# Performance work log

Hardware: AMD Instinct MI355X
Metric: run time of the kernel (lower is better)

The kernel has to match this reference:

```python
import jax, jax.numpy as jnp
import numpy as np

B, M, D = 2048, 40, 64          # batch, num fields, embedding dim
HIDDEN = [128, 128, 128]        # CIN layer sizes


def setup_inputs() -> dict:
    key = jax.random.key(0)
    kx, k0, k1, k2 = jax.random.split(key, 4)
    x = jax.random.normal(kx, (B, M, D), dtype=jnp.float32)
    # torch.rand -> uniform [0, 1)
    W0 = jax.random.uniform(k0, (M, M, HIDDEN[0]), dtype=jnp.float32)
    W1 = jax.random.uniform(k1, (M, HIDDEN[0], HIDDEN[1]), dtype=jnp.float32)
    W2 = jax.random.uniform(k2, (M, HIDDEN[1], HIDDEN[2]), dtype=jnp.float32)
    return {"x": x, "W0": W0, "W1": W1, "W2": W2}


def _cin_forward(x, Ws):
    # x: [b, m, d]. Each layer k:
    #   x_next[b, l, d] = sum_{m, h} x0[b, m, d] * x_k[b, h, d] * W_k[m, h, l]
    # which equals the torch 'bil,bjl->bjil' outer product followed by
    # 'bijk,ijl->bkl' + transpose, but expressed as one fused contraction
    # (opt_einsum picks a path avoiding the worst intermediate).
    ps = []
    xk = x  # [b, H_k, d], H_0 = m
    for W in Ws:
        x_next = jnp.einsum('bmd,bhd,mhl->bld', x, xk, W)  # [b, L_k, d]
        ps.append(jnp.sum(x_next, axis=2))                  # [b, L_k]
        xk = x_next
    return jnp.concatenate(ps, axis=1)                      # [b, sum(L_k)]


def reference(x, W0, W1, W2):
    return _cin_forward(x, (W0, W1, W2))
```

## Files before the change

kernel.cpp:

```cpp
#include <hip/hip_runtime.h>
#include <hip/hip_bf16.h>
#include <cstdint>

#define BATCH 2048
#define MF    40
#define DDIM  64
#define LDIM  128
#define ROWS  (BATCH * DDIM)

typedef __attribute__((ext_vector_type(4)))  short    short4_t;
typedef __attribute__((ext_vector_type(8)))  short    short8;
typedef __attribute__((ext_vector_type(8)))  __bf16   bf16x8;
typedef __attribute__((ext_vector_type(2)))  float    floatx2;
typedef __attribute__((ext_vector_type(16))) float    floatx16;

__device__ __forceinline__ unsigned short f32_to_bf16(float f) {
    union { float f; uint32_t u; } v; v.f = f;
    uint32_t u = v.u;
    uint32_t r = (u + 0x7fffu + ((u >> 16) & 1u)) >> 16;
    return (unsigned short)r;
}

__device__ __forceinline__ void barrier_raw() {
    asm volatile("s_barrier" ::: "memory");
}
__device__ __forceinline__ void lgkmwait0() {
    asm volatile("s_waitcnt lgkmcnt(0)" ::: "memory");
}
template <int N> __device__ __forceinline__ void vmwait() {
    if constexpr (N == 0)  asm volatile("s_waitcnt vmcnt(0)"  ::: "memory");
    if constexpr (N == 4)  asm volatile("s_waitcnt vmcnt(4)"  ::: "memory");
    if constexpr (N == 6)  asm volatile("s_waitcnt vmcnt(6)"  ::: "memory");
    if constexpr (N == 10) asm volatile("s_waitcnt vmcnt(10)" ::: "memory");
}

__global__ void k_wprep_all(const float* __restrict__ W0, const float* __restrict__ W1,
                            const float* __restrict__ W2,
                            unsigned short* __restrict__ W0t,
                            unsigned short* __restrict__ W1t,
                            unsigned short* __restrict__ W2t) {
    int bi = blockIdx.x;
    const float* W; unsigned short* Wt; int KK, H;
    if (bi < 640)       { W = W0; Wt = W0t; KK = 4; H = 40; }
    else if (bi < 1920) { bi -= 640;  W = W1; Wt = W1t; KK = 8; H = 128; }
    else                { bi -= 1920; W = W2; Wt = W2t; KK = 8; H = 128; }
    int lane = threadIdx.x;
    int cb = bi & 3;
    int mkk = bi >> 2;
    int kk = mkk % KK, m = mkk / KK;
    int l = cb * 32 + (lane & 31);
    int hbase = kk * 16 + (lane >> 5) * 8;
    unsigned short o[8];
#pragma unroll
    for (int j = 0; j < 8; ++j) {
        int h = hbase + j;
        float v = (h < H) ? W[((size_t)m * H + h) * LDIM + l] : 0.f;
        o[j] = f32_to_bf16(v);
    }
    *(short8*)(Wt + (((size_t)(m * KK + kk) * 4 + cb) * 64 + lane) * 8) = *(const short8*)o;
}

template <int KK>
__device__ __forceinline__ void layer_loop(
    const unsigned short* __restrict__ Wt,
    const float* __restrict__ x, int b,
    int lane, int hf, int r31, int cbg0, int cbg1,
    unsigned short* slabf,
    bf16x8 (&xk)[2][8], floatx16 (&acc)[2][2])
{
    constexpr int UPM  = KK / 4;
    constexpr int NU   = MF * UPM;
    constexpr int GATE = (KK == 8) ? 10 : 6;

    auto stage = [&](int uu) {
        int u = uu < NU ? uu : NU - 1;
        const unsigned short* src = Wt + (size_t)u * 8192;
        const int tid = threadIdx.x;
#pragma unroll
        for (int it = 0; it < 4; ++it) {
            int c = it * 256 + tid;
            __builtin_amdgcn_global_load_lds(
                (const __attribute__((address_space(1))) uint32_t*)(src + (size_t)c * 8),
                (__attribute__((address_space(3))) uint32_t*)(&slabf[(size_t)(u & 3) * 8192 + (size_t)c * 8]),
                16, 0, 0);
        }
    };
    auto ldfrag = [&](int u, int frag, int cb) {
        return __builtin_bit_cast(bf16x8, *(const short8*)(
            &slabf[(size_t)(u & 3) * 8192 + ((size_t)(frag * 4 + cb) * 64 + lane) * 8]));
    };

    acc[0][0] = floatx16{}; acc[0][1] = floatx16{};
    acc[1][0] = floatx16{}; acc[1][1] = floatx16{};

    vmwait<0>();
    stage(0); stage(1); stage(2);
    vmwait<4>();
    barrier_raw();

    bf16x8 bbuf[2][2];
#pragma unroll
    for (int p = 0; p < 2; ++p) {
        bbuf[p][0] = ldfrag(0, p, cbg0);
        bbuf[p][1] = ldfrag(0, p, cbg1);
    }

    float s0v = 0.f, s1v = 0.f;

#pragma unroll 1
    for (int m = 0; m < MF; ++m) {
        floatx16 P[2][2] = {};
#pragma unroll
        for (int kk = 0; kk < KK; ++kk) {
            if (kk % 4 == 0) {
                barrier_raw();
                asm volatile("s_setprio 1");
                if (kk == 0) {
                    const float* sp = x + ((size_t)b * MF + m) * DDIM + r31;
                    s0v = sp[0];
                    s1v = sp[32];
                }
                stage(m * UPM + kk / 4 + 3);
            }
            const int slot = kk & 1;
            P[0][0] = __builtin_amdgcn_mfma_f32_32x32x16_bf16(bbuf[slot][0], xk[0][kk], P[0][0], 0, 0, 0);
            P[1][0] = __builtin_amdgcn_mfma_f32_32x32x16_bf16(bbuf[slot][0], xk[1][kk], P[1][0], 0, 0, 0);
            P[0][1] = __builtin_amdgcn_mfma_f32_32x32x16_bf16(bbuf[slot][1], xk[0][kk], P[0][1], 0, 0, 0);
            P[1][1] = __builtin_amdgcn_mfma_f32_32x32x16_bf16(bbuf[slot][1], xk[1][kk], P[1][1], 0, 0, 0);
            {
                const int j  = kk + 2;
                int mm = m + ((j >= KK) ? 1 : 0);
                if (mm > MF - 1) mm = MF - 1;
                const int jj = (j >= KK) ? (j - KK) : j;
                const int u  = mm * UPM + jj / 4;
                bbuf[slot][0] = ldfrag(u, jj % 4, cbg0);
                bbuf[slot][1] = ldfrag(u, jj % 4, cbg1);
            }
            if (kk % 4 == 3) vmwait<GATE>();
        }
        asm volatile("s_setprio 0");
#pragma unroll
        for (int t = 0; t < 2; ++t) {
            const float sv = (t == 0) ? s0v : s1v;
            floatx2 s2 = {sv, sv};
#pragma unroll
            for (int cbp = 0; cbp < 2; ++cbp) {
                floatx2*       A = (floatx2*)&acc[t][cbp];
                const floatx2* Q = (const floatx2*)&P[t][cbp];
#pragma unroll
                for (int i = 0; i < 8; ++i) A[i] += s2 * Q[i];
            }
        }
    }
}

__global__ __launch_bounds__(256, 2) void k_cin(
    const float* __restrict__ x,
    const unsigned short* __restrict__ W0t,
    const unsigned short* __restrict__ W1t,
    const unsigned short* __restrict__ W2t,
    float* __restrict__ out)
{
    __shared__ unsigned short slab[4][8192];
    unsigned short* slabf = &slab[0][0];

    const int tid  = threadIdx.x;
    const int lane = tid & 63, wave = tid >> 6;
    const int hf   = lane >> 5, r31 = lane & 31;
    const int rowhalf = wave >> 1, colhalf = wave & 1;
    const int b = blockIdx.x * 2 + rowhalf;
    const int cbg0 = colhalf * 2, cbg1 = colhalf * 2 + 1;

    bf16x8   xk[2][8];
    floatx16 acc[2][2];

    auto write_ps = [&](int OFF) {
#pragma unroll
        for (int cbp = 0; cbp < 2; ++cbp) {
#pragma unroll
            for (int j = 0; j < 16; ++j) {
                float v = acc[0][cbp][j] + acc[1][cbp][j];
                v += __shfl_xor(v, 16);
                v += __shfl_xor(v, 8);
                v += __shfl_xor(v, 4);
                v += __shfl_xor(v, 2);
                v += __shfl_xor(v, 1);
                if (r31 == 0)
                    out[(size_t)b * 384 + OFF + (colhalf * 2 + cbp) * 32 +
                        (j & 3) + 8 * (j >> 2) + 4 * hf] = v;
            }
        }
    };

    auto exchange = [&]() {
        vmwait<0>();
        barrier_raw();
#pragma unroll
        for (int t = 0; t < 2; ++t)
#pragma unroll
            for (int cbp = 0; cbp < 2; ++cbp)
#pragma unroll
                for (int g = 0; g < 4; ++g) {
                    unsigned short o[4];
#pragma unroll
                    for (int i = 0; i < 4; ++i) o[i] = f32_to_bf16(acc[t][cbp][g * 4 + i]);
                    const int kk  = colhalf * 4 + cbp * 2 + (g >> 1);
                    const int hfr = g & 1;
                    *(short4_t*)(&slabf[(size_t)rowhalf * 8192 +
                        ((size_t)(t * 8 + kk) * 64 + hfr * 32 + r31) * 8 + 4 * hf]) =
                        *(const short4_t*)o;
                }
        lgkmwait0();
        barrier_raw();
#pragma unroll
        for (int t = 0; t < 2; ++t)
#pragma unroll
            for (int kk = 0; kk < 8; ++kk)
                xk[t][kk] = __builtin_bit_cast(bf16x8, *(const short8*)(
                    &slabf[(size_t)rowhalf * 8192 + ((size_t)(t * 8 + kk) * 64 + lane) * 8]));
        lgkmwait0();
        barrier_raw();
    };

#pragma unroll
    for (int t = 0; t < 2; ++t)
#pragma unroll
        for (int kk = 0; kk < 4; ++kk) {
            unsigned short tmp[8];
#pragma unroll
            for (int j = 0; j < 8; ++j) {
                int h = kk * 16 + hf * 8 + j;
                float v = (h < MF) ? x[((size_t)b * MF + h) * DDIM + t * 32 + r31] : 0.f;
                tmp[j] = f32_to_bf16(v);
            }
            xk[t][kk] = __builtin_bit_cast(bf16x8, *(const short8*)tmp);
        }

    layer_loop<4>(W0t, x, b, lane, hf, r31, cbg0, cbg1, slabf, xk, acc);
    write_ps(0);
    exchange();

    layer_loop<8>(W1t, x, b, lane, hf, r31, cbg0, cbg1, slabf, xk, acc);
    write_ps(128);
    exchange();

    layer_loop<8>(W2t, x, b, lane, hf, r31, cbg0, cbg1, slabf, xk, acc);
    write_ps(256);
}

extern "C" void kernel_launch(void* const* d_in, const int* in_sizes, int n_in,
                              void* d_out, int out_size, void* d_ws, size_t ws_size,
                              hipStream_t stream) {
    const float* x  = (const float*)d_in[0];
    const float* W0 = (const float*)d_in[1];
    const float* W1 = (const float*)d_in[2];
    const float* W2 = (const float*)d_in[3];
    float* out = (float*)d_out;

    char* ws = (char*)d_ws;
    size_t off = 0;
    auto alloc = [&](size_t bytes) -> void* {
        void* p = ws + off;
        off += (bytes + 255) & ~(size_t)255;
        return p;
    };
    unsigned short* W0t = (unsigned short*)alloc((size_t)MF * 4 * 2048 * 2);
    unsigned short* W1t = (unsigned short*)alloc((size_t)MF * 8 * 2048 * 2);
    unsigned short* W2t = (unsigned short*)alloc((size_t)MF * 8 * 2048 * 2);

    k_wprep_all<<<3200, 64, 0, stream>>>(W0, W1, W2, W0t, W1t, W2t);
    k_cin<<<ROWS / 128, 256, 0, stream>>>(x, W0t, W1t, W2t, out);
}
```

Measured before the change: 434.1 us.

## Split work to one batch per block across d-halves, shrink LDS staging

Each block now handles a single batch row, with its four waves split over the two 32-wide d-halves and two column groups, where before each block covered two batch rows. Per-wave accumulators and xk registers are halved and the LDS weight slab shrinks to 4096 entries per stage, so launch bounds can rise to four blocks per CU. Partial sums from the two d-halves are combined through a small shared scratch before the output is written. Each block still streams the full weights, so weight traffic through L2 per batch row doubles, and pipeline waits and barriers now come twice as often per unit of MFMA work.

```diff
diff --git a/kernel.cpp b/kernel.cpp
--- a/kernel.cpp
+++ b/kernel.cpp
@@ -6,7 +6,6 @@
 #define MF    40
 #define DDIM  64
 #define LDIM  128
-#define ROWS  (BATCH * DDIM)
 
 typedef __attribute__((ext_vector_type(4)))  short    short4_t;
 typedef __attribute__((ext_vector_type(8)))  short    short8;
@@ -28,10 +27,9 @@
     asm volatile("s_waitcnt lgkmcnt(0)" ::: "memory");
 }
 template <int N> __device__ __forceinline__ void vmwait() {
-    if constexpr (N == 0)  asm volatile("s_waitcnt vmcnt(0)"  ::: "memory");
-    if constexpr (N == 4)  asm volatile("s_waitcnt vmcnt(4)"  ::: "memory");
-    if constexpr (N == 6)  asm volatile("s_waitcnt vmcnt(6)"  ::: "memory");
-    if constexpr (N == 10) asm volatile("s_waitcnt vmcnt(10)" ::: "memory");
+    if constexpr (N == 0) asm volatile("s_waitcnt vmcnt(0)" ::: "memory");
+    if constexpr (N == 2) asm volatile("s_waitcnt vmcnt(2)" ::: "memory");
+    if constexpr (N == 3) asm volatile("s_waitcnt vmcnt(3)" ::: "memory");
 }
 
 __global__ void k_wprep_all(const float* __restrict__ W0, const float* __restrict__ W1,
@@ -63,39 +61,37 @@
 template <int KK>
 __device__ __forceinline__ void layer_loop(
     const unsigned short* __restrict__ Wt,
-    const float* __restrict__ x, int b,
-    int lane, int hf, int r31, int cbg0, int cbg1,
+    const float* __restrict__ x, int b, int t,
+    int lane, int cbg0, int cbg1,
     unsigned short* slabf,
-    bf16x8 (&xk)[2][8], floatx16 (&acc)[2][2])
+    bf16x8 (&xk)[8], floatx16 (&acc)[2])
 {
-    constexpr int UPM  = KK / 4;
-    constexpr int NU   = MF * UPM;
-    constexpr int GATE = (KK == 8) ? 10 : 6;
+    constexpr int UPM = KK / 2;
+    constexpr int NU  = MF * UPM;
 
     auto stage = [&](int uu) {
         int u = uu < NU ? uu : NU - 1;
-        const unsigned short* src = Wt + (size_t)u * 8192;
+        const unsigned short* src = Wt + (size_t)u * 4096;
         const int tid = threadIdx.x;
 #pragma unroll
-        for (int it = 0; it < 4; ++it) {
+        for (int it = 0; it < 2; ++it) {
             int c = it * 256 + tid;
             __builtin_amdgcn_global_load_lds(
                 (const __attribute__((address_space(1))) uint32_t*)(src + (size_t)c * 8),
-                (__attribute__((address_space(3))) uint32_t*)(&slabf[(size_t)(u & 3) * 8192 + (size_t)c * 8]),
+                (__attribute__((address_space(3))) uint32_t*)(&slabf[(u & 3) * 4096 + c * 8]),
                 16, 0, 0);
         }
     };
-    auto ldfrag = [&](int u, int frag, int cb) {
+    auto ldfrag = [&](int u, int f, int cb) {
         return __builtin_bit_cast(bf16x8, *(const short8*)(
-            &slabf[(size_t)(u & 3) * 8192 + ((size_t)(frag * 4 + cb) * 64 + lane) * 8]));
-    };
-
-    acc[0][0] = floatx16{}; acc[0][1] = floatx16{};
-    acc[1][0] = floatx16{}; acc[1][1] = floatx16{};
+            &slabf[(u & 3) * 4096 + ((f * 4 + cb) * 64 + lane) * 8]));
+    };
+
+    acc[0] = floatx16{}; acc[1] = floatx16{};
 
     vmwait<0>();
     stage(0); stage(1); stage(2);
-    vmwait<4>();
+    vmwait<2>();
     barrier_raw();
 
     bf16x8 bbuf[2][2];
@@ -105,146 +101,136 @@
         bbuf[p][1] = ldfrag(0, p, cbg1);
     }
 
-    float s0v = 0.f, s1v = 0.f;
+    float sv = 0.f;
 
 #pragma unroll 1
     for (int m = 0; m < MF; ++m) {
-        floatx16 P[2][2] = {};
+        floatx16 P[2] = {};
 #pragma unroll
         for (int kk = 0; kk < KK; ++kk) {
-            if (kk % 4 == 0) {
+            if ((kk & 1) == 0) {
                 barrier_raw();
                 asm volatile("s_setprio 1");
-                if (kk == 0) {
-                    const float* sp = x + ((size_t)b * MF + m) * DDIM + r31;
-                    s0v = sp[0];
-                    s1v = sp[32];
-                }
-                stage(m * UPM + kk / 4 + 3);
+                if (kk == 0)
+                    sv = x[((size_t)b * MF + m) * DDIM + t * 32 + (lane & 31)];
+                stage(m * UPM + (kk >> 1) + 3);
             }
             const int slot = kk & 1;
-            P[0][0] = __builtin_amdgcn_mfma_f32_32x32x16_bf16(bbuf[slot][0], xk[0][kk], P[0][0], 0, 0, 0);
-            P[1][0] = __builtin_amdgcn_mfma_f32_32x32x16_bf16(bbuf[slot][0], xk[1][kk], P[1][0], 0, 0, 0);
-            P[0][1] = __builtin_amdgcn_mfma_f32_32x32x16_bf16(bbuf[slot][1], xk[0][kk], P[0][1], 0, 0, 0);
-            P[1][1] = __builtin_amdgcn_mfma_f32_32x32x16_bf16(bbuf[slot][1], xk[1][kk], P[1][1], 0, 0, 0);
+            P[0] = __builtin_amdgcn_mfma_f32_32x32x16_bf16(bbuf[slot][0], xk[kk], P[0], 0, 0, 0);
+            P[1] = __builtin_amdgcn_mfma_f32_32x32x16_bf16(bbuf[slot][1], xk[kk], P[1], 0, 0, 0);
             {
                 const int j  = kk + 2;
                 int mm = m + ((j >= KK) ? 1 : 0);
                 if (mm > MF - 1) mm = MF - 1;
                 const int jj = (j >= KK) ? (j - KK) : j;
-                const int u  = mm * UPM + jj / 4;
-                bbuf[slot][0] = ldfrag(u, jj % 4, cbg0);
-                bbuf[slot][1] = ldfrag(u, jj % 4, cbg1);
-            }
-            if (kk % 4 == 3) vmwait<GATE>();
+                const int u  = mm * UPM + (jj >> 1);
+                bbuf[slot][0] = ldfrag(u, jj & 1, cbg0);
+                bbuf[slot][1] = ldfrag(u, jj & 1, cbg1);
+            }
+            if ((kk & 1) == 1) {
+                if (kk == 1) vmwait<3>(); else vmwait<2>();
+            }
         }
         asm volatile("s_setprio 0");
 #pragma unroll
-        for (int t = 0; t < 2; ++t) {
-            const float sv = (t == 0) ? s0v : s1v;
+        for (int cbp = 0; cbp < 2; ++cbp) {
             floatx2 s2 = {sv, sv};
-#pragma unroll
-            for (int cbp = 0; cbp < 2; ++cbp) {
-                floatx2*       A = (floatx2*)&acc[t][cbp];
-                const floatx2* Q = (const floatx2*)&P[t][cbp];
-#pragma unroll
-                for (int i = 0; i < 8; ++i) A[i] += s2 * Q[i];
-            }
-        }
-    }
-}
-
-__global__ __launch_bounds__(256, 2) void k_cin(
+            floatx2*       A = (floatx2*)&acc[cbp];
+            const floatx2* Q = (const floatx2*)&P[cbp];
+#pragma unroll
+            for (int i = 0; i < 8; ++i) A[i] += s2 * Q[i];
+        }
+    }
+}
+
+__global__ __launch_bounds__(256, 4) void k_cin(
     const float* __restrict__ x,
     const unsigned short* __restrict__ W0t,
     const unsigned short* __restrict__ W1t,
     const unsigned short* __restrict__ W2t,
     float* __restrict__ out)
 {
-    __shared__ unsigned short slab[4][8192];
+    __shared__ unsigned short slab[4][4096];
+    __shared__ float pscr[2][128];
     unsigned short* slabf = &slab[0][0];
 
     const int tid  = threadIdx.x;
     const int lane = tid & 63, wave = tid >> 6;
     const int hf   = lane >> 5, r31 = lane & 31;
-    const int rowhalf = wave >> 1, colhalf = wave & 1;
-    const int b = blockIdx.x * 2 + rowhalf;
-    const int cbg0 = colhalf * 2, cbg1 = colhalf * 2 + 1;
-
-    bf16x8   xk[2][8];
-    floatx16 acc[2][2];
+    const int t = wave >> 1, c = wave & 1;
+    const int b = blockIdx.x;
+    const int cbg0 = c * 2, cbg1 = c * 2 + 1;
+
+    bf16x8   xk[8];
+    floatx16 acc[2];
 
     auto write_ps = [&](int OFF) {
 #pragma unroll
         for (int cbp = 0; cbp < 2; ++cbp) {
 #pragma unroll
             for (int j = 0; j < 16; ++j) {
-                float v = acc[0][cbp][j] + acc[1][cbp][j];
+                float v = acc[cbp][j];
                 v += __shfl_xor(v, 16);
                 v += __shfl_xor(v, 8);
                 v += __shfl_xor(v, 4);
                 v += __shfl_xor(v, 2);
                 v += __shfl_xor(v, 1);
                 if (r31 == 0)
-                    out[(size_t)b * 384 + OFF + (colhalf * 2 + cbp) * 32 +
-                        (j & 3) + 8 * (j >> 2) + 4 * hf] = v;
-            }
-        }
+                    pscr[t][(c * 2 + cbp) * 32 + (j & 3) + 8 * (j >> 2) + 4 * hf] = v;
+            }
+        }
+        lgkmwait0();
+        barrier_raw();
+        if (tid < 128)
+            out[(size_t)b * 384 + OFF + tid] = pscr[0][tid] + pscr[1][tid];
     };
 
     auto exchange = [&]() {
         vmwait<0>();
         barrier_raw();
 #pragma unroll
-        for (int t = 0; t < 2; ++t)
-#pragma unroll
-            for (int cbp = 0; cbp < 2; ++cbp)
-#pragma unroll
-                for (int g = 0; g < 4; ++g) {
-                    unsigned short o[4];
-#pragma unroll
-                    for (int i = 0; i < 4; ++i) o[i] = f32_to_bf16(acc[t][cbp][g * 4 + i]);
-                    const int kk  = colhalf * 4 + cbp * 2 + (g >> 1);
-                    const int hfr = g & 1;
-                    *(short4_t*)(&slabf[(size_t)rowhalf * 8192 +
-                        ((size_t)(t * 8 + kk) * 64 + hfr * 32 + r31) * 8 + 4 * hf]) =
-                        *(const short4_t*)o;
-                }
+        for (int cbp = 0; cbp < 2; ++cbp)
+#pragma unroll
+            for (int g = 0; g < 4; ++g) {
+                unsigned short o[4];
+#pragma unroll
+                for (int i = 0; i < 4; ++i) o[i] = f32_to_bf16(acc[cbp][g * 4 + i]);
+                const int kk  = c * 4 + cbp * 2 + (g >> 1);
+                const int hfr = g & 1;
+                *(short4_t*)(&slabf[((t * 8 + kk) * 64 + hfr * 32 + r31) * 8 + 4 * hf]) =
+                    *(const short4_t*)o;
+            }
         lgkmwait0();
         barrier_raw();
 #pragma unroll
-        for (int t = 0; t < 2; ++t)
-#pragma unroll
-            for (int kk = 0; kk < 8; ++kk)
-                xk[t][kk] = __builtin_bit_cast(bf16x8, *(const short8*)(
-                    &slabf[(size_t)rowhalf * 8192 + ((size_t)(t * 8 + kk) * 64 + lane) * 8]));
+        for (int kk = 0; kk < 8; ++kk)
+            xk[kk] = __builtin_bit_cast(bf16x8, *(const short8*)(
+                &slabf[((t * 8 + kk) * 64 + lane) * 8]));
         lgkmwait0();
         barrier_raw();
     };
 
 #pragma unroll
-    for (int t = 0; t < 2; ++t)
-#pragma unroll
-        for (int kk = 0; kk < 4; ++kk) {
-            unsigned short tmp[8];
-#pragma unroll
-            for (int j = 0; j < 8; ++j) {
-                int h = kk * 16 + hf * 8 + j;
-                float v = (h < MF) ? x[((size_t)b * MF + h) * DDIM + t * 32 + r31] : 0.f;
-                tmp[j] = f32_to_bf16(v);
-            }
-            xk[t][kk] = __builtin_bit_cast(bf16x8, *(const short8*)tmp);
-        }
-
-    layer_loop<4>(W0t, x, b, lane, hf, r31, cbg0, cbg1, slabf, xk, acc);
+    for (int kk = 0; kk < 4; ++kk) {
+        unsigned short tmp[8];
+#pragma unroll
+        for (int j = 0; j < 8; ++j) {
+            int h = kk * 16 + hf * 8 + j;
+            float v = (h < MF) ? x[((size_t)b * MF + h) * DDIM + t * 32 + r31] : 0.f;
+            tmp[j] = f32_to_bf16(v);
+        }
+        xk[kk] = __builtin_bit_cast(bf16x8, *(const short8*)tmp);
+    }
+
+    layer_loop<4>(W0t, x, b, t, lane, cbg0, cbg1, slabf, xk, acc);
     write_ps(0);
     exchange();
 
-    layer_loop<8>(W1t, x, b, lane, hf, r31, cbg0, cbg1, slabf, xk, acc);
+    layer_loop<8>(W1t, x, b, t, lane, cbg0, cbg1, slabf, xk, acc);
     write_ps(128);
     exchange();
 
-    layer_loop<8>(W2t, x, b, lane, hf, r31, cbg0, cbg1, slabf, xk, acc);
+    layer_loop<8>(W2t, x, b, t, lane, cbg0, cbg1, slabf, xk, acc);
     write_ps(256);
 }
 
@@ -269,5 +255,5 @@
     unsigned short* W2t = (unsigned short*)alloc((size_t)MF * 8 * 2048 * 2);
 
     k_wprep_all<<<3200, 64, 0, stream>>>(W0, W1, W2, W0t, W1t, W2t);
-    k_cin<<<ROWS / 128, 256, 0, stream>>>(x, W0t, W1t, W2t, out);
-}
+    k_cin<<<BATCH, 256, 0, stream>>>(x, W0t, W1t, W2t, out);
+}
```

Result: slower. 520.6 us (+19.9%).
